# Kernel optimization log

Hardware: AMD Instinct MI355X
Metric: run time of the kernel (lower is better)

Reference implementation:

```python
import jax, jax.numpy as jnp
import numpy as np

N, E, D, H, C = 50000, 800000, 128, 4, 32  # nodes, edges, in/out dim, heads, head dim
NEG_SLOPE = 0.2
LN_EPS = 1e-5
NORM_EPS = 1e-12


def setup_inputs() -> dict:
    key = jax.random.key(0)
    ks = jax.random.split(key, 10)
    s = 1.0 / np.sqrt(D)
    return {
        "x": jax.random.normal(ks[0], (N, D), dtype=jnp.float32),
        "edge_index": jax.random.randint(ks[1], (2, E), 0, N, dtype=jnp.int64),
        "gamma": 1.0 + 0.1 * jax.random.normal(ks[2], (D,), dtype=jnp.float32),
        "beta": 0.1 * jax.random.normal(ks[3], (D,), dtype=jnp.float32),
        "W_l": jax.random.normal(ks[4], (D, H * C), dtype=jnp.float32) * s,
        "b_l": jnp.zeros((H * C,), dtype=jnp.float32),
        "W_r": jax.random.normal(ks[5], (D, H * C), dtype=jnp.float32) * s,
        "b_r": jnp.zeros((H * C,), dtype=jnp.float32),
        "att": jax.random.normal(ks[6], (H, C), dtype=jnp.float32) * s,
        "bias": jnp.zeros((H * C,), dtype=jnp.float32),
        "scale": jnp.array(1.0, dtype=jnp.float32),
    }


def reference(x, edge_index, gamma, beta, W_l, b_l, W_r, b_r, att, bias, scale):
    n = x.shape[0]
    # Pre-activation: LayerNorm -> ReLU (dropout=0 in eval)
    mu = jnp.mean(x, axis=-1, keepdims=True)
    var = jnp.mean(jnp.square(x - mu), axis=-1, keepdims=True)
    h = jax.nn.relu((x - mu) / jnp.sqrt(var + LN_EPS) * gamma + beta)

    # GATv2Conv (PyG defaults: add_self_loops=True, negative_slope=0.2)
    loops = jnp.arange(n, dtype=edge_index.dtype)
    src = jnp.concatenate([edge_index[0], loops])  # message source j
    dst = jnp.concatenate([edge_index[1], loops])  # message target i

    xl = (h @ W_l + b_l).reshape(n, H, C)
    xr = (h @ W_r + b_r).reshape(n, H, C)

    # per-edge GATv2 score: a^T LeakyReLU(xl[j] + xr[i])  -> [E2, H]
    feat = jax.nn.leaky_relu(xl[src] + xr[dst], NEG_SLOPE)
    e = jnp.einsum('ehc,hc->eh', feat, att)

    # segment softmax over incoming edges of each target node
    m = jax.ops.segment_max(e, dst, num_segments=n)
    p = jnp.exp(e - m[dst])
    denom = jax.ops.segment_sum(p, dst, num_segments=n)
    alpha = p / denom[dst]  # [E2, H]

    # scatter-aggregate weighted source features
    msg = alpha[:, :, None] * xl[src]  # [E2, H, C]
    out = jax.ops.segment_sum(msg, dst, num_segments=n).reshape(n, H * C) + bias

    # MsgNorm: normalize(msg) * ||h||_2 * scale
    out_norm = jnp.sqrt(jnp.sum(jnp.square(out), axis=-1, keepdims=True))
    msg_n = out / jnp.maximum(out_norm, NORM_EPS)
    h_norm = jnp.sqrt(jnp.sum(jnp.square(h), axis=-1, keepdims=True))
    gat_out = msg_n * h_norm * scale

    # residual (projection is None since in_channels == out_channels)
    return x + gat_out
```

## Files before the change

### kernel.cpp

```cpp
#include <hip/hip_runtime.h>
#include <hip/hip_bf16.h>
#include <math.h>

#define N_NODES 50000
#define N_EDGES 800000
#define E2 (N_EDGES + N_NODES)
#define D 128

#define NB_LN 12500
#define NB_W 128

#define BSHIFT 8
#define NBUCK 196
#define SCHUNK 4096
#define NB_SC ((E2 + SCHUNK - 1) / SCHUNK)
#define NB_GEMM (((N_NODES + 127) / 128) * 2)

typedef short short8 __attribute__((ext_vector_type(8)));
typedef float f32x4 __attribute__((ext_vector_type(4)));
typedef _Float16 h16x2 __attribute__((ext_vector_type(2)));
typedef _Float16 h16x8 __attribute__((ext_vector_type(8)));

__device__ __forceinline__ float waveReduceSum(float v) {
#pragma unroll
  for (int off = 32; off >= 1; off >>= 1) v += __shfl_xor(v, off);
  return v;
}

__device__ __forceinline__ h16x2 shfl_xor_h2(h16x2 v, int off) {
  int r = __shfl_xor(__builtin_bit_cast(int, v), off);
  return __builtin_bit_cast(h16x2, r);
}

__global__ void __launch_bounds__(256) k_pre(
    const float* __restrict__ x, const float* __restrict__ gamma,
    const float* __restrict__ beta, const float* __restrict__ Wl,
    const float* __restrict__ Wr, const int* __restrict__ ei,
    __hip_bfloat16* __restrict__ hb, float* __restrict__ hnorm,
    __hip_bfloat16* __restrict__ Wt, int* __restrict__ bcnt) {
  const int b = blockIdx.x;
  if (b < NB_LN) {
    int wid = threadIdx.x >> 6;
    int lane = threadIdx.x & 63;
    int i = b * 4 + wid;
    const float2 xv = *(const float2*)&x[(size_t)i * D + lane * 2];
    float s = waveReduceSum(xv.x + xv.y);
    float mean = s * (1.0f / D);
    float d0 = xv.x - mean, d1 = xv.y - mean;
    float vs = waveReduceSum(d0 * d0 + d1 * d1);
    float rstd = rsqrtf(vs * (1.0f / D) + 1e-5f);
    const float2 g = *(const float2*)&gamma[lane * 2];
    const float2 bb = *(const float2*)&beta[lane * 2];
    float h0 = fmaxf(d0 * rstd * g.x + bb.x, 0.0f);
    float h1 = fmaxf(d1 * rstd * g.y + bb.y, 0.0f);
    __hip_bfloat162 hv;
    hv.x = __float2bfloat16(h0);
    hv.y = __float2bfloat16(h1);
    *(__hip_bfloat162*)&hb[(size_t)i * D + lane * 2] = hv;
    float ns = waveReduceSum(h0 * h0 + h1 * h1);
    if (lane == 0) hnorm[i] = sqrtf(ns);
  } else if (b < NB_LN + NB_W) {
    int local = b - NB_LN;
    int n = local * 2 + (threadIdx.x >> 7);
    int k = threadIdx.x & 127;
    float v = (n < D) ? Wl[(size_t)k * D + n] : Wr[(size_t)k * D + (n - D)];
    Wt[n * D + k] = __float2bfloat16(v);
  } else {
    __shared__ int c[256];
    const int t = threadIdx.x;
    c[t] = 0;
    __syncthreads();
    const int s0 = (b - NB_LN - NB_W) * SCHUNK;
#pragma unroll
    for (int k = 0; k < 16; ++k) {
      int e = s0 + t + k * 256;
      if (e < E2) {
        int dst = (e < N_EDGES) ? ei[N_EDGES + e] : (e - N_EDGES);
        atomicAdd(&c[dst >> BSHIFT], 1);
      }
    }
    __syncthreads();
    if (c[t]) atomicAdd(&bcnt[t], c[t]);
  }
}

__global__ void __launch_bounds__(256) k_bscatter(const int* __restrict__ ei,
                                                  const int* __restrict__ bcnt,
                                                  int* __restrict__ cnt0,
                                                  int2* __restrict__ bucketed) {
  __shared__ int c[256], base[256], sd[256];
  const int t = threadIdx.x;
  const int own = (t < NBUCK) ? bcnt[t] : 0;
  sd[t] = own;
  c[t] = 0;
  __syncthreads();
  for (int off = 1; off < 256; off <<= 1) {
    int u = 0;
    if (t >= off) u = sd[t - off];
    __syncthreads();
    if (t >= off) sd[t] += u;
    __syncthreads();
  }
  const int boffL = sd[t] - own;
  const int s0 = blockIdx.x * SCHUNK;
#pragma unroll
  for (int k = 0; k < 16; ++k) {
    int e = s0 + t + k * 256;
    if (e < E2) {
      int dst = (e < N_EDGES) ? ei[N_EDGES + e] : (e - N_EDGES);
      atomicAdd(&c[dst >> BSHIFT], 1);
    }
  }
  __syncthreads();
  if (t < NBUCK) {
    base[t] = c[t] ? (boffL + atomicAdd(&cnt0[t], c[t])) : 0;
    c[t] = 0;
  }
  __syncthreads();
#pragma unroll
  for (int k = 0; k < 16; ++k) {
    int e = s0 + t + k * 256;
    if (e < E2) {
      int src, dst;
      if (e < N_EDGES) {
        src = ei[e];
        dst = ei[N_EDGES + e];
      } else {
        src = dst = e - N_EDGES;
      }
      int bk = dst >> BSHIFT;
      int pos = base[bk] + atomicAdd(&c[bk], 1);
      bucketed[pos] = make_int2(src, dst);
    }
  }
}

__global__ void __launch_bounds__(256) k_mid(
    const int2* __restrict__ bucketed, const int* __restrict__ bcnt,
    int* __restrict__ rowptr, int* __restrict__ csr,
    const __hip_bfloat16* __restrict__ hb, const __hip_bfloat16* __restrict__ Wt,
    const float* __restrict__ bL, const float* __restrict__ bR,
    _Float16* __restrict__ xlh, _Float16* __restrict__ xrh) {
  __shared__ char smem[65536];
  const int t = threadIdx.x;
  if (blockIdx.x < NBUCK) {
    int* cnt = (int*)smem;
    int* tsum = cnt + 256;
    int* cursor = tsum + 256;
    int* red = cursor + 256;
    const int b = blockIdx.x;
    const int base = b << BSHIFT;
    const int nnode = min(256, N_NODES - base);
    red[t] = (t < b) ? bcnt[t] : 0;
    cnt[t] = 0;
    __syncthreads();
    for (int off = 128; off >= 1; off >>= 1) {
      if (t < off) red[t] += red[t + off];
      __syncthreads();
    }
    const int e0 = red[0], e1 = red[0] + bcnt[b];
    if (b == 0 && t == 0) rowptr[N_NODES] = E2;
    for (int e = e0 + t; e < e1; e += 256) {
      int2 pr = bucketed[e];
      atomicAdd(&cnt[pr.y - base], 1);
    }
    __syncthreads();
    const int own = cnt[t];
    tsum[t] = own;
    __syncthreads();
    for (int off = 1; off < 256; off <<= 1) {
      int u = 0;
      if (t >= off) u = tsum[t - off];
      __syncthreads();
      if (t >= off) tsum[t] += u;
      __syncthreads();
    }
    const int ebase = e0 + tsum[t] - own;
    cursor[t] = ebase;
    if (t < nnode) rowptr[base + t] = ebase;
    __syncthreads();
    for (int e = e0 + t; e < e1; e += 256) {
      int2 pr = bucketed[e];
      int pos = atomicAdd(&cursor[pr.y - base], 1);
      csr[pos] = pr.x;
    }
  } else {
    unsigned short* As = (unsigned short*)smem;
    unsigned short* Bs = As + 128 * 128;
    const int bid = blockIdx.x - NBUCK;
    const int row0 = (bid >> 1) * 128;
    const int nhalf = bid & 1;
    const unsigned short* hu = (const unsigned short*)hb;
    const unsigned short* wu = (const unsigned short*)Wt;
#pragma unroll
    for (int it = 0; it < 8; ++it) {
      int idx = t + it * 256;
      int r = idx >> 4, g = idx & 15;
      int gs = g ^ (r & 15);
      short8 av = {};
      int grow = row0 + r;
      if (grow < N_NODES) av = *(const short8*)&hu[(size_t)grow * D + g * 8];
      *(short8*)&As[r * 128 + gs * 8] = av;
      short8 bv = *(const short8*)&wu[(size_t)(nhalf * 128 + r) * D + g * 8];
      *(short8*)&Bs[r * 128 + gs * 8] = bv;
    }
    __syncthreads();
    const int w = t >> 6, lane = t & 63;
    const int wm = (w >> 1) * 64, wn = (w & 1) * 64;
    const int lr = lane & 15, lq = lane >> 4;
    f32x4 acc[4][4] = {};
#pragma unroll
    for (int kb = 0; kb < 4; ++kb) {
      short8 af[4], bfr[4];
#pragma unroll
      for (int mi = 0; mi < 4; ++mi) {
        int r = wm + mi * 16 + lr;
        int g = (kb * 4 + lq) ^ (r & 15);
        af[mi] = *(const short8*)&As[r * 128 + g * 8];
      }
#pragma unroll
      for (int ni = 0; ni < 4; ++ni) {
        int r = wn + ni * 16 + lr;
        int g = (kb * 4 + lq) ^ (r & 15);
        bfr[ni] = *(const short8*)&Bs[r * 128 + g * 8];
      }
#pragma unroll
      for (int mi = 0; mi < 4; ++mi)
#pragma unroll
        for (int ni = 0; ni < 4; ++ni)
          acc[mi][ni] = __builtin_amdgcn_mfma_f32_16x16x32_bf16(af[mi], bfr[ni],
                                                                acc[mi][ni], 0, 0, 0);
    }
    const float* bb = (nhalf == 0) ? bL : bR;
    _Float16* dst = (nhalf == 0) ? xlh : xrh;
#pragma unroll
    for (int mi = 0; mi < 4; ++mi) {
#pragma unroll
      for (int ni = 0; ni < 4; ++ni) {
#pragma unroll
        for (int r = 0; r < 4; ++r) {
          int row = row0 + wm + mi * 16 + lq * 4 + r;
          int col = wn + ni * 16 + lr;
          if (row < N_NODES)
            dst[(size_t)row * D + col] = (_Float16)(acc[mi][ni][r] + bb[col]);
        }
      }
    }
  }
}

__global__ void __launch_bounds__(256) k_node(
    const float* __restrict__ x, const _Float16* __restrict__ xlh,
    const _Float16* __restrict__ xrh, const float* __restrict__ hnorm,
    const int* __restrict__ rowptr, const int* __restrict__ csr,
    const float* __restrict__ att, const float* __restrict__ bias,
    const float* __restrict__ scale, float* __restrict__ out) {
  const int wid = threadIdx.x >> 6;
  const int lane = threadIdx.x & 63;
  const int i = blockIdx.x * 4 + wid;
  if (i >= N_NODES) return;
  const int g = lane >> 4;
  const int q = lane & 15;

  const h16x8 xrv = *(const h16x8*)(xrh + (size_t)i * D + q * 8);
  h16x2 xr2[4], at2[4];
  {
    const float4 a0 = *(const float4*)&att[q * 8];
    const float4 a1 = *(const float4*)&att[q * 8 + 4];
    at2[0] = (h16x2){(_Float16)a0.x, (_Float16)a0.y};
    at2[1] = (h16x2){(_Float16)a0.z, (_Float16)a0.w};
    at2[2] = (h16x2){(_Float16)a1.x, (_Float16)a1.y};
    at2[3] = (h16x2){(_Float16)a1.z, (_Float16)a1.w};
#pragma unroll
    for (int z = 0; z < 4; ++z) xr2[z] = (h16x2){xrv[2 * z], xrv[2 * z + 1]};
  }
  const h16x2 c02 = {(_Float16)0.2f, (_Float16)0.2f};

  const int e0 = rowptr[i], e1 = rowptr[i + 1];
  h16x2 A2[4] = {};
  float S = 0.f;

  int ja = csr[min(e0 + g, e1 - 1)];
  h16x8 r0 = *(const h16x8*)(xlh + (size_t)ja * D + q * 8);
  int jb = csr[min(e0 + 4 + g, e1 - 1)];
  h16x8 r1 = *(const h16x8*)(xlh + (size_t)jb * D + q * 8);
  int jc = csr[min(e0 + 8 + g, e1 - 1)];
  h16x8 r2 = *(const h16x8*)(xlh + (size_t)jc * D + q * 8);
  int jd = csr[min(e0 + 12 + g, e1 - 1)];

  for (int e = e0; e < e1; e += 4) {
    const h16x8 cur = r0;
    r0 = r1;
    r1 = r2;
    r2 = *(const h16x8*)(xlh + (size_t)jd * D + q * 8);
    jd = csr[min(e + 16 + g, e1 - 1)];
    const bool ok = (e + g) < e1;

    h16x2 v2[4];
    v2[0] = (h16x2){cur[0], cur[1]};
    v2[1] = (h16x2){cur[2], cur[3]};
    v2[2] = (h16x2){cur[4], cur[5]};
    v2[3] = (h16x2){cur[6], cur[7]};
    float sc = 0.f;
#pragma unroll
    for (int z = 0; z < 4; ++z) {
      h16x2 f = v2[z] + xr2[z];
      h16x2 lf = __builtin_elementwise_max(f, f * c02);
      sc = __builtin_amdgcn_fdot2(lf, at2[z], sc, false);
    }
    sc += __shfl_xor(sc, 1);
    sc += __shfl_xor(sc, 2);
    const float p = ok ? __expf(sc) : 0.f;
    S += p;
    const _Float16 ph = (_Float16)p;
    const h16x2 p2 = {ph, ph};
#pragma unroll
    for (int z = 0; z < 4; ++z) A2[z] = v2[z] * p2 + A2[z];
  }

#pragma unroll
  for (int off = 16; off <= 32; off <<= 1) {
#pragma unroll
    for (int z = 0; z < 4; ++z) A2[z] = A2[z] + shfl_xor_h2(A2[z], off);
    S += __shfl_xor(S, off);
  }

  const float si = 1.0f / S;
  float o[8];
  float b8[8];
  *(float4*)&b8[0] = *(const float4*)&bias[q * 8];
  *(float4*)&b8[4] = *(const float4*)&bias[q * 8 + 4];
  float dot = 0.f;
#pragma unroll
  for (int z = 0; z < 4; ++z) {
    o[2 * z] = fmaf((float)A2[z][0], si, b8[2 * z]);
    o[2 * z + 1] = fmaf((float)A2[z][1], si, b8[2 * z + 1]);
    dot = fmaf(o[2 * z], o[2 * z], dot);
    dot = fmaf(o[2 * z + 1], o[2 * z + 1], dot);
  }
  const float nrm = sqrtf(waveReduceSum(dot) * 0.25f);
  const float gg = hnorm[i] * scale[0] / fmaxf(nrm, 1e-12f);

  if (lane < 16) {
    float x8[8];
    *(float4*)&x8[0] = *(const float4*)&x[(size_t)i * D + q * 8];
    *(float4*)&x8[4] = *(const float4*)&x[(size_t)i * D + q * 8 + 4];
    float r8[8];
#pragma unroll
    for (int z = 0; z < 8; ++z) r8[z] = fmaf(o[z], gg, x8[z]);
    *(float4*)&out[(size_t)i * D + q * 8] = *(float4*)&r8[0];
    *(float4*)&out[(size_t)i * D + q * 8 + 4] = *(float4*)&r8[4];
  }
}

extern "C" void kernel_launch(void* const* d_in, const int* in_sizes, int n_in,
                              void* d_out, int out_size, void* d_ws, size_t ws_size,
                              hipStream_t stream) {
  const float* x = (const float*)d_in[0];
  const int* ei = (const int*)d_in[1];
  const float* gamma = (const float*)d_in[2];
  const float* beta = (const float*)d_in[3];
  const float* Wl = (const float*)d_in[4];
  const float* bL = (const float*)d_in[5];
  const float* Wr = (const float*)d_in[6];
  const float* bR = (const float*)d_in[7];
  const float* att = (const float*)d_in[8];
  const float* bias = (const float*)d_in[9];
  const float* scale = (const float*)d_in[10];
  float* out = (float*)d_out;

  int2* bucketed = (int2*)d_ws;
  int* csr = (int*)(bucketed + E2);
  int* rowptr = csr + E2;
  int* bcnt = rowptr + N_NODES + 16;
  int* cnt0 = bcnt + 256;
  float* hnorm = (float*)(cnt0 + 256);
  __hip_bfloat16* hb = (__hip_bfloat16*)(hnorm + N_NODES);
  __hip_bfloat16* Wt = hb + (size_t)N_NODES * D;
  _Float16* xlh = (_Float16*)(Wt + 256 * D);
  _Float16* xrh = xlh + (size_t)N_NODES * D;

  hipMemsetAsync(bcnt, 0, 512 * sizeof(int), stream);
  k_pre<<<NB_LN + NB_W + NB_SC, 256, 0, stream>>>(x, gamma, beta, Wl, Wr, ei, hb,
                                                  hnorm, Wt, bcnt);
  k_bscatter<<<NB_SC, 256, 0, stream>>>(ei, bcnt, cnt0, bucketed);
  k_mid<<<NBUCK + NB_GEMM, 256, 0, stream>>>(bucketed, bcnt, rowptr, csr, hb, Wt,
                                             bL, bR, xlh, xrh);
  k_node<<<(N_NODES + 3) / 4, 256, 0, stream>>>(x, xlh, xrh, hnorm, rowptr, csr, att,
                                                bias, scale, out);
}
```

Baseline: 116.7 us.

## Co-schedule bucket scatter with GEMM and simplify edge-loop addressing

Moves the GEMM blocks out of the CSR-build kernel so they run in the same launch as the bucket scatter, and gives the CSR fine build its own small kernel. This lets the GEMM overlap the scatter work instead of the CSR pass. In the node kernel, the per-iteration min-clamped CSR index is dropped in favour of 32-bit byte offsets, relying on a zeroed 32-entry pad after the CSR array so reads past the end stay in bounds. The attention vector is pre-scaled by log2(e) so exp2 can replace exp.

```diff
diff --git a/kernel.cpp b/kernel.cpp
--- a/kernel.cpp
+++ b/kernel.cpp
@@ -84,110 +84,65 @@
   }
 }
 
-__global__ void __launch_bounds__(256) k_bscatter(const int* __restrict__ ei,
-                                                  const int* __restrict__ bcnt,
-                                                  int* __restrict__ cnt0,
-                                                  int2* __restrict__ bucketed) {
-  __shared__ int c[256], base[256], sd[256];
-  const int t = threadIdx.x;
-  const int own = (t < NBUCK) ? bcnt[t] : 0;
-  sd[t] = own;
-  c[t] = 0;
-  __syncthreads();
-  for (int off = 1; off < 256; off <<= 1) {
-    int u = 0;
-    if (t >= off) u = sd[t - off];
-    __syncthreads();
-    if (t >= off) sd[t] += u;
-    __syncthreads();
-  }
-  const int boffL = sd[t] - own;
-  const int s0 = blockIdx.x * SCHUNK;
-#pragma unroll
-  for (int k = 0; k < 16; ++k) {
-    int e = s0 + t + k * 256;
-    if (e < E2) {
-      int dst = (e < N_EDGES) ? ei[N_EDGES + e] : (e - N_EDGES);
-      atomicAdd(&c[dst >> BSHIFT], 1);
-    }
-  }
-  __syncthreads();
-  if (t < NBUCK) {
-    base[t] = c[t] ? (boffL + atomicAdd(&cnt0[t], c[t])) : 0;
-    c[t] = 0;
-  }
-  __syncthreads();
-#pragma unroll
-  for (int k = 0; k < 16; ++k) {
-    int e = s0 + t + k * 256;
-    if (e < E2) {
-      int src, dst;
-      if (e < N_EDGES) {
-        src = ei[e];
-        dst = ei[N_EDGES + e];
-      } else {
-        src = dst = e - N_EDGES;
-      }
-      int bk = dst >> BSHIFT;
-      int pos = base[bk] + atomicAdd(&c[bk], 1);
-      bucketed[pos] = make_int2(src, dst);
-    }
-  }
-}
-
-__global__ void __launch_bounds__(256) k_mid(
-    const int2* __restrict__ bucketed, const int* __restrict__ bcnt,
-    int* __restrict__ rowptr, int* __restrict__ csr,
+__global__ void __launch_bounds__(256) k_A(
+    const int* __restrict__ ei, const int* __restrict__ bcnt,
+    int* __restrict__ cnt0, int2* __restrict__ bucketed,
     const __hip_bfloat16* __restrict__ hb, const __hip_bfloat16* __restrict__ Wt,
     const float* __restrict__ bL, const float* __restrict__ bR,
     _Float16* __restrict__ xlh, _Float16* __restrict__ xrh) {
   __shared__ char smem[65536];
   const int t = threadIdx.x;
-  if (blockIdx.x < NBUCK) {
-    int* cnt = (int*)smem;
-    int* tsum = cnt + 256;
-    int* cursor = tsum + 256;
-    int* red = cursor + 256;
-    const int b = blockIdx.x;
-    const int base = b << BSHIFT;
-    const int nnode = min(256, N_NODES - base);
-    red[t] = (t < b) ? bcnt[t] : 0;
-    cnt[t] = 0;
-    __syncthreads();
-    for (int off = 128; off >= 1; off >>= 1) {
-      if (t < off) red[t] += red[t + off];
-      __syncthreads();
-    }
-    const int e0 = red[0], e1 = red[0] + bcnt[b];
-    if (b == 0 && t == 0) rowptr[N_NODES] = E2;
-    for (int e = e0 + t; e < e1; e += 256) {
-      int2 pr = bucketed[e];
-      atomicAdd(&cnt[pr.y - base], 1);
-    }
-    __syncthreads();
-    const int own = cnt[t];
-    tsum[t] = own;
+  if (blockIdx.x < NB_SC) {
+    int* c = (int*)smem;
+    int* base = c + 256;
+    int* sd = base + 256;
+    const int own = (t < NBUCK) ? bcnt[t] : 0;
+    sd[t] = own;
+    c[t] = 0;
     __syncthreads();
     for (int off = 1; off < 256; off <<= 1) {
       int u = 0;
-      if (t >= off) u = tsum[t - off];
+      if (t >= off) u = sd[t - off];
       __syncthreads();
-      if (t >= off) tsum[t] += u;
+      if (t >= off) sd[t] += u;
       __syncthreads();
     }
-    const int ebase = e0 + tsum[t] - own;
-    cursor[t] = ebase;
-    if (t < nnode) rowptr[base + t] = ebase;
-    __syncthreads();
-    for (int e = e0 + t; e < e1; e += 256) {
-      int2 pr = bucketed[e];
-      int pos = atomicAdd(&cursor[pr.y - base], 1);
-      csr[pos] = pr.x;
+    const int boffL = sd[t] - own;
+    const int s0 = blockIdx.x * SCHUNK;
+#pragma unroll
+    for (int k = 0; k < 16; ++k) {
+      int e = s0 + t + k * 256;
+      if (e < E2) {
+        int dst = (e < N_EDGES) ? ei[N_EDGES + e] : (e - N_EDGES);
+        atomicAdd(&c[dst >> BSHIFT], 1);
+      }
+    }
+    __syncthreads();
+    if (t < NBUCK) {
+      base[t] = c[t] ? (boffL + atomicAdd(&cnt0[t], c[t])) : 0;
+      c[t] = 0;
+    }
+    __syncthreads();
+#pragma unroll
+    for (int k = 0; k < 16; ++k) {
+      int e = s0 + t + k * 256;
+      if (e < E2) {
+        int src, dst;
+        if (e < N_EDGES) {
+          src = ei[e];
+          dst = ei[N_EDGES + e];
+        } else {
+          src = dst = e - N_EDGES;
+        }
+        int bk = dst >> BSHIFT;
+        int pos = base[bk] + atomicAdd(&c[bk], 1);
+        bucketed[pos] = make_int2(src, dst);
+      }
     }
   } else {
     unsigned short* As = (unsigned short*)smem;
     unsigned short* Bs = As + 128 * 128;
-    const int bid = blockIdx.x - NBUCK;
+    const int bid = blockIdx.x - NB_SC;
     const int row0 = (bid >> 1) * 128;
     const int nhalf = bid & 1;
     const unsigned short* hu = (const unsigned short*)hb;
@@ -246,6 +201,53 @@
         }
       }
     }
+  }
+}
+
+__global__ void __launch_bounds__(256) k_B(const int2* __restrict__ bucketed,
+                                           const int* __restrict__ bcnt,
+                                           int* __restrict__ rowptr,
+                                           int* __restrict__ csr) {
+  __shared__ int cnt[256], tsum[256], cursor[256], red[256];
+  const int b = blockIdx.x;
+  const int base = b << BSHIFT;
+  const int nnode = min(256, N_NODES - base);
+  const int t = threadIdx.x;
+  red[t] = (t < b) ? bcnt[t] : 0;
+  cnt[t] = 0;
+  __syncthreads();
+  for (int off = 128; off >= 1; off >>= 1) {
+    if (t < off) red[t] += red[t + off];
+    __syncthreads();
+  }
+  const int e0 = red[0], e1 = red[0] + bcnt[b];
+  if (b == 0) {
+    if (t == 0) rowptr[N_NODES] = E2;
+    if (t < 32) csr[E2 + t] = 0;
+  }
+  for (int e = e0 + t; e < e1; e += 256) {
+    int2 pr = bucketed[e];
+    atomicAdd(&cnt[pr.y - base], 1);
+  }
+  __syncthreads();
+  const int own = cnt[t];
+  tsum[t] = own;
+  __syncthreads();
+  for (int off = 1; off < 256; off <<= 1) {
+    int u = 0;
+    if (t >= off) u = tsum[t - off];
+    __syncthreads();
+    if (t >= off) tsum[t] += u;
+    __syncthreads();
+  }
+  const int ebase = e0 + tsum[t] - own;
+  cursor[t] = ebase;
+  if (t < nnode) rowptr[base + t] = ebase;
+  __syncthreads();
+  for (int e = e0 + t; e < e1; e += 256) {
+    int2 pr = bucketed[e];
+    int pos = atomicAdd(&cursor[pr.y - base], 1);
+    csr[pos] = pr.x;
   }
 }
 
@@ -265,12 +267,13 @@
   const h16x8 xrv = *(const h16x8*)(xrh + (size_t)i * D + q * 8);
   h16x2 xr2[4], at2[4];
   {
+    const float LOG2E = 1.44269504f;
     const float4 a0 = *(const float4*)&att[q * 8];
     const float4 a1 = *(const float4*)&att[q * 8 + 4];
-    at2[0] = (h16x2){(_Float16)a0.x, (_Float16)a0.y};
-    at2[1] = (h16x2){(_Float16)a0.z, (_Float16)a0.w};
-    at2[2] = (h16x2){(_Float16)a1.x, (_Float16)a1.y};
-    at2[3] = (h16x2){(_Float16)a1.z, (_Float16)a1.w};
+    at2[0] = (h16x2){(_Float16)(a0.x * LOG2E), (_Float16)(a0.y * LOG2E)};
+    at2[1] = (h16x2){(_Float16)(a0.z * LOG2E), (_Float16)(a0.w * LOG2E)};
+    at2[2] = (h16x2){(_Float16)(a1.x * LOG2E), (_Float16)(a1.y * LOG2E)};
+    at2[3] = (h16x2){(_Float16)(a1.z * LOG2E), (_Float16)(a1.w * LOG2E)};
 #pragma unroll
     for (int z = 0; z < 4; ++z) xr2[z] = (h16x2){xrv[2 * z], xrv[2 * z + 1]};
   }
@@ -280,20 +283,26 @@
   h16x2 A2[4] = {};
   float S = 0.f;
 
-  int ja = csr[min(e0 + g, e1 - 1)];
-  h16x8 r0 = *(const h16x8*)(xlh + (size_t)ja * D + q * 8);
-  int jb = csr[min(e0 + 4 + g, e1 - 1)];
-  h16x8 r1 = *(const h16x8*)(xlh + (size_t)jb * D + q * 8);
-  int jc = csr[min(e0 + 8 + g, e1 - 1)];
-  h16x8 r2 = *(const h16x8*)(xlh + (size_t)jc * D + q * 8);
-  int jd = csr[min(e0 + 12 + g, e1 - 1)];
+  const char* csrB = (const char*)csr;
+  const char* xB = (const char*)xlh;
+  const unsigned qofs = (unsigned)q * 16;
+  unsigned coff = (unsigned)(e0 + g) << 2;
+
+  int ja = *(const int*)(csrB + coff);
+  int jb = *(const int*)(csrB + coff + 16);
+  int jc = *(const int*)(csrB + coff + 32);
+  int jd = *(const int*)(csrB + coff + 48);
+  h16x8 r0 = *(const h16x8*)(xB + (((unsigned)ja << 8) + qofs));
+  h16x8 r1 = *(const h16x8*)(xB + (((unsigned)jb << 8) + qofs));
+  h16x8 r2 = *(const h16x8*)(xB + (((unsigned)jc << 8) + qofs));
 
   for (int e = e0; e < e1; e += 4) {
     const h16x8 cur = r0;
     r0 = r1;
     r1 = r2;
-    r2 = *(const h16x8*)(xlh + (size_t)jd * D + q * 8);
-    jd = csr[min(e + 16 + g, e1 - 1)];
+    r2 = *(const h16x8*)(xB + (((unsigned)jd << 8) + qofs));
+    coff += 16;
+    jd = *(const int*)(csrB + coff + 48);
     const bool ok = (e + g) < e1;
 
     h16x2 v2[4];
@@ -310,7 +319,7 @@
     }
     sc += __shfl_xor(sc, 1);
     sc += __shfl_xor(sc, 2);
-    const float p = ok ? __expf(sc) : 0.f;
+    const float p = ok ? __builtin_exp2f(sc) : 0.f;
     S += p;
     const _Float16 ph = (_Float16)p;
     const h16x2 p2 = {ph, ph};
@@ -371,7 +380,7 @@
 
   int2* bucketed = (int2*)d_ws;
   int* csr = (int*)(bucketed + E2);
-  int* rowptr = csr + E2;
+  int* rowptr = csr + E2 + 32;
   int* bcnt = rowptr + N_NODES + 16;
   int* cnt0 = bcnt + 256;
   float* hnorm = (float*)(cnt0 + 256);
@@ -383,9 +392,9 @@
   hipMemsetAsync(bcnt, 0, 512 * sizeof(int), stream);
   k_pre<<<NB_LN + NB_W + NB_SC, 256, 0, stream>>>(x, gamma, beta, Wl, Wr, ei, hb,
                                                   hnorm, Wt, bcnt);
-  k_bscatter<<<NB_SC, 256, 0, stream>>>(ei, bcnt, cnt0, bucketed);
-  k_mid<<<NBUCK + NB_GEMM, 256, 0, stream>>>(bucketed, bcnt, rowptr, csr, hb, Wt,
-                                             bL, bR, xlh, xrh);
+  k_A<<<NB_SC + NB_GEMM, 256, 0, stream>>>(ei, bcnt, cnt0, bucketed, hb, Wt, bL, bR,
+                                           xlh, xrh);
+  k_B<<<NBUCK, 256, 0, stream>>>(bucketed, bcnt, rowptr, csr);
   k_node<<<(N_NODES + 3) / 4, 256, 0, stream>>>(x, xlh, xrh, hnorm, rowptr, csr, att,
                                                 bias, scale, out);
 }
```

Result: slower. 123.5 us (+5.8%).
